# Optimization experiments

Hardware: AMD Instinct MI355X
Metric: run time of the kernel (lower is better)

Reference implementation:

```python
import jax, jax.numpy as jnp
import numpy as np
import math

B, L, D, H = 2, 2048, 1024, 16
d = D // H

def setup_inputs() -> dict:
    key = jax.random.key(0)
    ks = jax.random.split(key, 12)
    s = 0.02
    return {
        "x": jax.random.normal(ks[0], (B, L, D), jnp.float32),
        "Wqkv_w": jax.random.normal(ks[1], (D, 3 * D), jnp.float32) * s,
        "Wqkv_b": jax.random.normal(ks[2], (3 * D,), jnp.float32) * s,
        "out_w": jax.random.normal(ks[3], (D, D), jnp.float32) * s,
        "out_b": jax.random.normal(ks[4], (D,), jnp.float32) * s,
        "W_static": jnp.zeros((H, d, d), jnp.float32),
        "Lambda_raw": jax.random.uniform(ks[5], (H, d, d), jnp.float32, -3.0, 3.0),
        "Gamma": jax.random.uniform(ks[6], (H, d, d), jnp.float32, -0.5 / math.sqrt(d), 0.5 / math.sqrt(d)),
        "gate_w1": jax.random.normal(ks[7], (D, D // 2), jnp.float32) * s,
        "gate_b1": jax.random.normal(ks[8], (D // 2,), jnp.float32) * s,
        "gate_w2": jax.random.normal(ks[9], (D // 2, H), jnp.float32) * s,
        "gate_b2": jax.random.normal(ks[10], (H,), jnp.float32) * s,
    }

def _forward(x, Wqkv_w, Wqkv_b, out_w, out_b, W_static, Lambda_raw, Gamma,
             gate_w1, gate_b1, gate_w2, gate_b2):
    scale = 1.0 / math.sqrt(d)
    qkv = x @ Wqkv_w + Wqkv_b                              # (B,L,3D)
    qkv = qkv.reshape(B, L, 3, H, d).transpose(2, 0, 3, 1, 4)  # (3,B,H,L,d)
    q, k, v = qkv[0], qkv[1], qkv[2]

    # --- causal softmax attention branch ---
    scores = jnp.einsum('bhid,bhjd->bhij', q, k) * scale
    mask = jnp.triu(jnp.full((L, L), -10000.0, scores.dtype), 1)
    attn = jax.nn.softmax(scores + mask, axis=-1)
    y_softmax = jnp.einsum('bhij,bhjd->bhid', attn, v)     # (B,H,L,d)

    # --- STP fast-weight branch: decaying Hebbian state recurrence ---
    k_stp = k * scale
    retention = 1.0 - jax.nn.sigmoid(Lambda_raw)           # (H,d,d)
    def step(state, qkv_t):
        q_t, k_t, v_t = qkv_t                              # each (B,H,d)
        hebbian = v_t[..., :, None] * k_t[..., None, :]    # (B,H,d,d)
        state = retention * state + Gamma * hebbian
        y_t = jnp.einsum('bhij,bhj->bhi', W_static + state, q_t)
        return state, y_t
    qkv_seq = (q.transpose(2, 0, 1, 3), k_stp.transpose(2, 0, 1, 3), v.transpose(2, 0, 1, 3))
    state0 = jnp.zeros((B, H, d, d), x.dtype)
    _, y_stp = jax.lax.scan(step, state0, qkv_seq)         # (L,B,H,d)
    y_stp = y_stp.transpose(1, 2, 0, 3)                    # (B,H,L,d)

    # --- learned gate ---
    h = jax.nn.gelu(x @ gate_w1 + gate_b1, approximate=False)
    alpha = jax.nn.sigmoid(h @ gate_w2 + gate_b2)          # (B,L,H)
    alpha = alpha.transpose(0, 2, 1)[..., None]            # (B,H,L,1)

    y = alpha * y_softmax + (1.0 - alpha) * y_stp          # (B,H,L,d)
    y = y.transpose(0, 2, 1, 3).reshape(B, L, D)
    return y @ out_w + out_b

def reference(x, Wqkv_w, Wqkv_b, out_w, out_b, W_static, Lambda_raw, Gamma,
              gate_w1, gate_b1, gate_w2, gate_b2):
    return _forward(x, Wqkv_w, Wqkv_b, out_w, out_b, W_static, Lambda_raw, Gamma,
                    gate_w1, gate_b1, gate_w2, gate_b2)
```

## Files before the change

kernel.cpp:

```cpp
#include <hip/hip_runtime.h>
#include <cstdint>
#include <cstddef>

#define B_ 2
#define L_ 2048
#define D_ 1024
#define H_ 16
#define DH 64

typedef __attribute__((ext_vector_type(8))) short bf16x8;
typedef __attribute__((ext_vector_type(4))) float f32x4;
typedef unsigned short u16;

__device__ inline u16 f2bf(float f) {
  unsigned u = __builtin_bit_cast(unsigned, f);
  u += 0x7fffu + ((u >> 16) & 1u);
  return (u16)(u >> 16);
}

__device__ inline float bf2f(u16 x) {
  return __builtin_bit_cast(float, (unsigned)x << 16);
}

template <int CTRL>
__device__ inline float dpp_mov(float x) {
  int t = __builtin_amdgcn_update_dpp(0, __builtin_bit_cast(int, x), CTRL, 0xf, 0xf, true);
  return __builtin_bit_cast(float, t);
}

#define GLDS16(ldst, gsrc)                                              \
  __builtin_amdgcn_global_load_lds(                                    \
      (const __attribute__((address_space(1))) void*)(gsrc),           \
      (__attribute__((address_space(3))) void*)(ldst), 16, 0, 0)

__device__ inline void stp_upd(float4& z, const float4 r, const float4 g,
                               const float4 wlc, float vv,
                               float kx, float ky, float kz, float kw) {
  z.x = fmaf(r.x, z.x, fmaf(g.x * vv, kx, wlc.x));
  z.y = fmaf(r.y, z.y, fmaf(g.y * vv, ky, wlc.y));
  z.z = fmaf(r.z, z.z, fmaf(g.z * vv, kz, wlc.z));
  z.w = fmaf(r.w, z.w, fmaf(g.w * vv, kw, wlc.w));
}

__device__ inline void stp_upd1(float4& z, const float4 r, const float4 g,
                                float vv, float kx, float ky, float kz, float kw) {
  z.x = fmaf(r.x, z.x, (g.x * vv) * kx);
  z.y = fmaf(r.y, z.y, (g.y * vv) * ky);
  z.z = fmaf(r.z, z.z, (g.z * vv) * kz);
  z.w = fmaf(r.w, z.w, (g.w * vv) * kw);
}

__device__ inline float stp_dot(const float4 z, float qx, float qy, float qz, float qw) {
  float p = z.x * qx;
  p = fmaf(z.y, qy, p);
  p = fmaf(z.z, qz, p);
  p = fmaf(z.w, qw, p);
  return p;
}

__device__ inline float dpp_red16(float p) {
  p = p + dpp_mov<0x128>(p);
  p = p + dpp_mov<0x124>(p);
  p = p + dpp_mov<0x122>(p);
  p = p + dpp_mov<0x121>(p);
  return p;
}


__device__ inline void d_transpose(const float* __restrict__ in,
                                   u16* __restrict__ out, int R, int C,
                                   int bx, int by, float tile[32][33], int tid) {
  const int tx = tid & 31, ty = tid >> 5;
  const int c0 = bx * 32, r0 = by * 32;
#pragma unroll
  for (int j = 0; j < 4; ++j)
    tile[ty + j * 8][tx] = in[(size_t)(r0 + ty + j * 8) * C + c0 + tx];
  __syncthreads();
#pragma unroll
  for (int j = 0; j < 4; ++j)
    out[(size_t)(c0 + ty + j * 8) * R + r0 + tx] = f2bf(tile[tx][ty + j * 8]);
}

__global__ __launch_bounds__(256) void prep_fused(
    const float* __restrict__ x, u16* __restrict__ xbf,
    const float* __restrict__ wqkv_w, u16* __restrict__ wqkvT,
    const float* __restrict__ out_w, u16* __restrict__ owT,
    const float* __restrict__ g_w1, u16* __restrict__ g1T,
    const float* __restrict__ lam, const float* __restrict__ gma,
    float* __restrict__ retb, float* __restrict__ gamb,
    float* __restrict__ retb64) {
  __shared__ float tile[32][33];
  const int bid = blockIdx.x, tid = threadIdx.x;
  if (bid < 4096) {
    int i = bid * 256 + tid;
    float4 v = ((const float4*)x)[i];
    ushort4 o;
    o.x = f2bf(v.x); o.y = f2bf(v.y); o.z = f2bf(v.z); o.w = f2bf(v.w);
    ((ushort4*)xbf)[i] = o;
  } else if (bid < 7168) {
    int r = bid - 4096;
    d_transpose(wqkv_w, wqkvT, 1024, 3072, r % 96, r / 96, tile, tid);
  } else if (bid < 8192) {
    int r = bid - 7168;
    d_transpose(out_w, owT, 1024, 1024, r % 32, r / 32, tile, tid);
  } else if (bid < 8704) {
    int r = bid - 8192;
    d_transpose(g_w1, g1T, 1024, 512, r % 16, r / 16, tile, tid);
  } else {
    int i = (bid - 8704) * 256 + tid;
    float l = lam[i];
    float r = 1.f / (1.f + expf(l));
    retb[i] = r;
    gamb[i] = gma[i] * 0.125f;
    float r2 = r * r;
    float r4 = r2 * r2;
    float r8 = r4 * r4;
    float r16 = r8 * r8;
    float r32 = r16 * r16;
    retb64[i] = r32 * r32;
  }
}


struct GemmP {
  const u16* A; const u16* Bt; int M, N, K;
  const float* bias;
  u16* qb; u16* kb; u16* vtb;
  float* hout;
  float* outp;
};

template <int EPI>
__device__ void gemm_body(const GemmP& p, int lin0, int nwgx, int nwgtot,
                          u16* As, u16* Bs, u16* tileT) {
  const int tid = threadIdx.x;
  const int lane = tid & 63;
  const int w = tid >> 6;
  const int wr = w >> 1, wc = w & 1;
  const int lr = lane & 15, lk = lane >> 4;
  const int cpx = nwgtot >> 3;
  const int lin = (lin0 & 7) * cpx + (lin0 >> 3);
  const int m0 = (lin / nwgx) * 128, n0 = (lin % nwgx) * 128;

  f32x4 acc[4][4];
#pragma unroll
  for (int i = 0; i < 4; ++i)
#pragma unroll
    for (int j = 0; j < 4; ++j) acc[i][j] = (f32x4){0.f, 0.f, 0.f, 0.f};

  for (int k0 = 0; k0 < p.K; k0 += 64) {
    __syncthreads();
#pragma unroll
    for (int it = 0; it < 4; ++it) {
      int idx = it * 256 + tid;
      int row = idx >> 3;
      int ch = (idx & 7) ^ (row & 7);
      GLDS16(&As[idx * 8], p.A + (size_t)(m0 + row) * p.K + k0 + ch * 8);
      GLDS16(&Bs[idx * 8], p.Bt + (size_t)(n0 + row) * p.K + k0 + ch * 8);
    }
    __syncthreads();
#pragma unroll
    for (int kk = 0; kk < 2; ++kk) {
      const int slot = ((kk * 4 + lk) ^ (lr & 7)) * 8;
      bf16x8 af[4], bfr[4];
#pragma unroll
      for (int mr = 0; mr < 4; ++mr)
        af[mr] = *(const bf16x8*)&As[(wr * 64 + mr * 16 + lr) * 64 + slot];
#pragma unroll
      for (int nr = 0; nr < 4; ++nr)
        bfr[nr] = *(const bf16x8*)&Bs[(wc * 64 + nr * 16 + lr) * 64 + slot];
#pragma unroll
      for (int mr = 0; mr < 4; ++mr)
#pragma unroll
        for (int nr = 0; nr < 4; ++nr)
          acc[mr][nr] = __builtin_amdgcn_mfma_f32_16x16x32_bf16(af[mr], bfr[nr], acc[mr][nr], 0, 0, 0);
    }
  }

  if constexpr (EPI == 0) {
    if (n0 < 2048) {
#pragma unroll
      for (int mr = 0; mr < 4; ++mr)
#pragma unroll
        for (int nr = 0; nr < 4; ++nr) {
          const int col = n0 + wc * 64 + nr * 16 + lr;
#pragma unroll
          for (int rr = 0; rr < 4; ++rr) {
            const int row = m0 + wr * 64 + mr * 16 + lk * 4 + rr;
            float v = acc[mr][nr][rr] + p.bias[col];
            int which = col >> 10, hh = (col >> 6) & 15, ii = col & 63;
            int b = row >> 11, ll = row & 2047;
            size_t bi = ((size_t)(b * 16 + hh) * L_ + ll) * 64 + ii;
            if (which == 0) p.qb[bi] = f2bf(v * 0.125f);
            else            p.kb[bi] = f2bf(v);
          }
        }
    } else {
#pragma unroll 1
      for (int h2 = 0; h2 < 2; ++h2) {
        __syncthreads();
        if (wr == h2) {
#pragma unroll
          for (int mr = 0; mr < 4; ++mr)
#pragma unroll
            for (int nr = 0; nr < 4; ++nr) {
              const int cl = wc * 64 + nr * 16 + lr;
              const float bv = p.bias[n0 + cl];
#pragma unroll
              for (int rr = 0; rr < 4; ++rr) {
                const int rl2 = mr * 16 + lk * 4 + rr;
                tileT[cl * 72 + rl2] = f2bf(acc[mr][nr][rr] + bv);
              }
            }
        }
        __syncthreads();
        const int c = tid >> 1, half = tid & 1;
        const int vcol = (n0 - 2048) + c;
        const int hh = vcol >> 6, ii = vcol & 63;
        const int b = m0 >> 11;
        const int ll0 = (m0 & 2047) + h2 * 64 + half * 32;
        u16* dst = p.vtb + ((size_t)(b * 16 + hh) * 64 + ii) * L_ + ll0;
        const u16* src = &tileT[c * 72 + half * 32];
#pragma unroll
        for (int k = 0; k < 4; ++k)
          *(int4*)(dst + k * 8) = *(const int4*)(src + k * 8);
      }
    }
  } else {
#pragma unroll
    for (int mr = 0; mr < 4; ++mr)
#pragma unroll
      for (int nr = 0; nr < 4; ++nr) {
        const int col = n0 + wc * 64 + nr * 16 + lr;
#pragma unroll
        for (int rr = 0; rr < 4; ++rr) {
          const int row = m0 + wr * 64 + mr * 16 + lk * 4 + rr;
          float v = acc[mr][nr][rr] + p.bias[col];
          if constexpr (EPI == 1) {
            float g = 0.5f * v * (1.f + erff(v * 0.70710678118f));
            p.hout[(size_t)row * p.N + col] = g;
          } else {
            p.outp[(size_t)row * p.N + col] = v;
          }
        }
      }
  }
}

__global__ __launch_bounds__(256, 4) void gemm01_kernel(GemmP p0, GemmP p1) {
  __shared__ u16 sbuf[16384];
  u16* As = sbuf;
  u16* Bs = sbuf + 8192;
  u16* tileT = sbuf;
  const int bid = blockIdx.x;
  if (bid < 768) gemm_body<0>(p0, bid, 24, 768, As, Bs, tileT);
  else           gemm_body<1>(p1, bid - 768, 4, 128, As, Bs, tileT);
}

__global__ __launch_bounds__(256, 4) void gemm2_kernel(GemmP p) {
  __shared__ u16 As[8192];
  __shared__ u16 Bs[8192];
  const int lin0 = (int)blockIdx.x + 8 * (int)blockIdx.y;
  gemm_body<2>(p, lin0, 8, 256, As, Bs, nullptr);
}


__global__ __launch_bounds__(256) void alpha_kernel(
    const float* __restrict__ hbuf, const float* __restrict__ w2,
    const float* __restrict__ b2, float* __restrict__ alp) {
  const int tid = threadIdx.x;
  const int row = blockIdx.x * 16 + (tid >> 4);
  const int n = tid & 15;
  const float4* h4 = (const float4*)(hbuf + (size_t)row * 512);
  float acc = 0.f;
#pragma unroll 2
  for (int kk = 0; kk < 128; ++kk) {
    float4 hv = h4[kk];
    acc = fmaf(hv.x, w2[(kk * 4 + 0) * 16 + n], acc);
    acc = fmaf(hv.y, w2[(kk * 4 + 1) * 16 + n], acc);
    acc = fmaf(hv.z, w2[(kk * 4 + 2) * 16 + n], acc);
    acc = fmaf(hv.w, w2[(kk * 4 + 3) * 16 + n], acc);
  }
  float z = acc + b2[n];
  alp[row * 16 + n] = 1.f / (1.f + __expf(-z));
}


__global__ __launch_bounds__(256, 2) void attn_kernel(
    const u16* __restrict__ qb, const u16* __restrict__ kb,
    const u16* __restrict__ vtb, float* __restrict__ ysm) {
  __shared__ u16 Ks[64 * 64];
  __shared__ u16 Vts[64 * 64];
  __shared__ u16 Pl[4][16 * 64];
  const int tid = threadIdx.x, lane = tid & 63, w = tid >> 6;
  const int lr = lane & 15, lk = lane >> 4;
  const int lin = (int)blockIdx.x + 16 * (int)blockIdx.y;
  const int bh = lin & 31;
  const int xp = lin >> 5;
  const int qtA = 31 - xp, qtB = xp;

  const u16* kbase0 = kb + (size_t)bh * (L_ * 64);
  const u16* vbase0 = vtb + (size_t)bh * (64 * L_);

  const size_t qbaseA = ((size_t)bh * L_ + qtA * 64 + w * 16 + lr) * 64;
  const size_t qbaseB = ((size_t)bh * L_ + qtB * 64 + w * 16 + lr) * 64;
  bf16x8 qfrA[2], qfrB[2];
  qfrA[0] = *(const bf16x8*)(qb + qbaseA + lk * 8);
  qfrA[1] = *(const bf16x8*)(qb + qbaseA + 32 + lk * 8);
  qfrB[0] = *(const bf16x8*)(qb + qbaseB + lk * 8);
  qfrB[1] = *(const bf16x8*)(qb + qbaseB + 32 + lk * 8);

  f32x4 yaccA[4], yaccB[4];
  float mrowA[4], lrowA[4], mrowB[4], lrowB[4];
#pragma unroll
  for (int i = 0; i < 4; ++i) {
    yaccA[i] = (f32x4){0.f, 0.f, 0.f, 0.f};
    yaccB[i] = (f32x4){0.f, 0.f, 0.f, 0.f};
    mrowA[i] = -1e30f; mrowB[i] = -1e30f;
    lrowA[i] = 0.f;    lrowB[i] = 0.f;
  }

  auto process = [&](const bf16x8* qfr, f32x4* yacc, float* mrow, float* lrow,
                     bool maskTile) {
    f32x4 s[4];
#pragma unroll
    for (int f = 0; f < 4; ++f) {
      f32x4 sf = (f32x4){0.f, 0.f, 0.f, 0.f};
#pragma unroll
      for (int ss = 0; ss < 2; ++ss) {
        bf16x8 kfr = *(const bf16x8*)&Ks[(f * 16 + lr) * 64 +
                                         (((ss * 4 + lk) ^ (lr & 7)) * 8)];
        sf = __builtin_amdgcn_mfma_f32_16x16x32_bf16(qfr[ss], kfr, sf, 0, 0, 0);
      }
      s[f] = sf;
    }
    if (maskTile) {
#pragma unroll
      for (int f = 0; f < 4; ++f)
#pragma unroll
        for (int rr = 0; rr < 4; ++rr)
          if (f * 16 + lr > w * 16 + lk * 4 + rr) s[f][rr] = -1e30f;
    }
    float mx[4];
#pragma unroll
    for (int rr = 0; rr < 4; ++rr) {
      float m = fmaxf(fmaxf(s[0][rr], s[1][rr]), fmaxf(s[2][rr], s[3][rr]));
      m = fmaxf(m, dpp_mov<0x128>(m));
      m = fmaxf(m, dpp_mov<0x124>(m));
      m = fmaxf(m, dpp_mov<0x122>(m));
      m = fmaxf(m, dpp_mov<0x121>(m));
      mx[rr] = m;
    }
    bool need = (mx[0] > mrow[0] + 8.f) | (mx[1] > mrow[1] + 8.f) |
                (mx[2] > mrow[2] + 8.f) | (mx[3] > mrow[3] + 8.f);
    if (__any(need)) {
#pragma unroll
      for (int rr = 0; rr < 4; ++rr) {
        float mn = fmaxf(mrow[rr], mx[rr]);
        float c = __expf(mrow[rr] - mn);
        lrow[rr] *= c;
#pragma unroll
        for (int nf = 0; nf < 4; ++nf) yacc[nf][rr] *= c;
        mrow[rr] = mn;
      }
    }
    u16* pw = &Pl[w][0];
#pragma unroll
    for (int rr = 0; rr < 4; ++rr) {
      const int prow = lk * 4 + rr;
      float rs = 0.f;
#pragma unroll
      for (int f = 0; f < 4; ++f) {
        float pv = __expf(s[f][rr] - mrow[rr]);
        rs += pv;
        int chunk = f * 2 + (lr >> 3);
        pw[prow * 64 + ((chunk ^ (prow & 7)) * 8) + (lr & 7)] = f2bf(pv);
      }
      rs = rs + dpp_mov<0x128>(rs);
      rs = rs + dpp_mov<0x124>(rs);
      rs = rs + dpp_mov<0x122>(rs);
      rs = rs + dpp_mov<0x121>(rs);
      lrow[rr] += rs;
    }
#pragma unroll
    for (int s2 = 0; s2 < 2; ++s2) {
      bf16x8 pa = *(const bf16x8*)&pw[lr * 64 + (((s2 * 4 + lk) ^ (lr & 7)) * 8)];
#pragma unroll
      for (int nf = 0; nf < 4; ++nf) {
        bf16x8 vfr = *(const bf16x8*)&Vts[(nf * 16 + lr) * 64 +
                                          (((s2 * 4 + lk) ^ (lr & 7)) * 8)];
        yacc[nf] = __builtin_amdgcn_mfma_f32_16x16x32_bf16(pa, vfr, yacc[nf], 0, 0, 0);
      }
    }
  };

  const int nkv = qtA + 1;
  for (int kt = 0; kt < nkv; ++kt) {
    const int kv0 = kt * 64;
    __syncthreads();
#pragma unroll
    for (int it = 0; it < 2; ++it) {
      int idx = it * 256 + tid;
      int row = idx >> 3, ch = idx & 7;
      int sch = (ch ^ (row & 7)) * 8;
      *(int4*)&Ks[row * 64 + sch] =
          *(const int4*)(kbase0 + (size_t)(kv0 + row) * 64 + ch * 8);
      *(int4*)&Vts[row * 64 + sch] =
          *(const int4*)(vbase0 + (size_t)row * L_ + kv0 + ch * 8);
    }
    __syncthreads();

    process(qfrA, yaccA, mrowA, lrowA, kt == qtA);
    if (kt <= qtB) process(qfrB, yaccB, mrowB, lrowB, kt == qtB);
  }

#pragma unroll
  for (int nf = 0; nf < 4; ++nf)
#pragma unroll
    for (int rr = 0; rr < 4; ++rr) {
      int rowl = w * 16 + lk * 4 + rr;
      int col = nf * 16 + lr;
      ysm[((size_t)bh * L_ + qtA * 64 + rowl) * 64 + col] = yaccA[nf][rr] / lrowA[rr];
      ysm[((size_t)bh * L_ + qtB * 64 + rowl) * 64 + col] = yaccB[nf][rr] / lrowB[rr];
    }
}


__global__ __launch_bounds__(256, 4) void stp_pass1(
    const u16* __restrict__ kb, const u16* __restrict__ vtb,
    const float* __restrict__ retb, const float* __restrict__ gamb,
    float* __restrict__ slocal) {
  __shared__ u16 Klds[4096];
  const int tid = threadIdx.x, lane = tid & 63, w = tid >> 6;
  const int bh = blockIdx.x >> 5, c = blockIdx.x & 31;
  const int hh = bh & 15;
  const int m = lane >> 4, j4 = (lane & 15) * 4;
  const int i0m = w * 16 + m * 4;

  const u16* kcb = kb + ((size_t)bh * L_ + c * 64) * 64;
  GLDS16(&Klds[tid * 8], kcb + tid * 8);
  GLDS16(&Klds[2048 + tid * 8], kcb + 2048 + tid * 8);
  __syncthreads();

  const int hij = (hh * 64 + i0m) * 64 + j4;
  const float4 r0 = *(const float4*)(retb + hij);
  const float4 r1 = *(const float4*)(retb + hij + 64);
  const float4 r2 = *(const float4*)(retb + hij + 128);
  const float4 r3 = *(const float4*)(retb + hij + 192);
  const float4 g0 = *(const float4*)(gamb + hij);
  const float4 g1 = *(const float4*)(gamb + hij + 64);
  const float4 g2 = *(const float4*)(gamb + hij + 128);
  const float4 g3 = *(const float4*)(gamb + hij + 192);
  const u16* vbp = vtb + ((size_t)bh * 64 + i0m) * L_ + c * 64;

  float4 s0 = {0,0,0,0}, s1 = {0,0,0,0}, s2 = {0,0,0,0}, s3 = {0,0,0,0};
#pragma unroll 1
  for (int t8 = 0; t8 < 8; ++t8) {
    const bf16x8 va = *(const bf16x8*)(vbp + t8 * 8);
    const bf16x8 vb = *(const bf16x8*)(vbp + L_ + t8 * 8);
    const bf16x8 vc = *(const bf16x8*)(vbp + 2 * L_ + t8 * 8);
    const bf16x8 vd = *(const bf16x8*)(vbp + 3 * L_ + t8 * 8);
#pragma unroll
    for (int tt = 0; tt < 8; ++tt) {
      const ushort4 k4u = *(const ushort4*)&Klds[(t8 * 8 + tt) * 64 + j4];
      const float kx = bf2f(k4u.x), ky = bf2f(k4u.y),
                  kz = bf2f(k4u.z), kw = bf2f(k4u.w);
      stp_upd1(s0, r0, g0, bf2f((u16)va[tt]), kx, ky, kz, kw);
      stp_upd1(s1, r1, g1, bf2f((u16)vb[tt]), kx, ky, kz, kw);
      stp_upd1(s2, r2, g2, bf2f((u16)vc[tt]), kx, ky, kz, kw);
      stp_upd1(s3, r3, g3, bf2f((u16)vd[tt]), kx, ky, kz, kw);
    }
  }
  float* sb = slocal + (((size_t)(bh * 32 + c) * 64) + i0m) * 64 + j4;
  *(float4*)(sb)       = s0;
  *(float4*)(sb + 64)  = s1;
  *(float4*)(sb + 128) = s2;
  *(float4*)(sb + 192) = s3;
}

__global__ __launch_bounds__(256) void stp_scan(
    const float* __restrict__ retb64, float* __restrict__ slocal) {
  const int idx = blockIdx.x * 256 + threadIdx.x;
  const int j = idx & 63, i1 = (idx >> 6) & 63, bh = idx >> 12;
  const int hh = bh & 15;
  const float r64 = retb64[(hh * 64 + i1) * 64 + j];
  float carry = 0.f;
  for (int c = 0; c < 32; ++c) {
    const size_t off = ((((size_t)bh * 32 + c) * 64 + i1) * 64 + j);
    const float sl = slocal[off];
    slocal[off] = carry;
    carry = fmaf(r64, carry, sl);
  }
}

__global__ __launch_bounds__(256, 4) void stp_pass2(
    const u16* __restrict__ qb, const u16* __restrict__ kb,
    const u16* __restrict__ vtb, const float* __restrict__ retb,
    const float* __restrict__ gamb, const float* __restrict__ wst,
    const float* __restrict__ slocal, float* __restrict__ ystp) {
  __shared__ u16 KQ[8192];
  const int tid = threadIdx.x, lane = tid & 63, w = tid >> 6;
  const int bh = blockIdx.x >> 5, c = blockIdx.x & 31;
  const int hh = bh & 15;
  const int m = lane >> 4, jc = lane & 15, j4 = jc * 4;
  const int i0m = w * 16 + m * 4;

  const size_t cb = ((size_t)bh * L_ + c * 64) * 64;
  GLDS16(&KQ[tid * 8], kb + cb + tid * 8);
  GLDS16(&KQ[2048 + tid * 8], kb + cb + 2048 + tid * 8);
  GLDS16(&KQ[4096 + tid * 8], qb + cb + tid * 8);
  GLDS16(&KQ[6144 + tid * 8], qb + cb + 2048 + tid * 8);
  __syncthreads();

  const int hij = (hh * 64 + i0m) * 64 + j4;
  const float4 r0 = *(const float4*)(retb + hij);
  const float4 r1 = *(const float4*)(retb + hij + 64);
  const float4 r2 = *(const float4*)(retb + hij + 128);
  const float4 r3 = *(const float4*)(retb + hij + 192);
  const float4 g0 = *(const float4*)(gamb + hij);
  const float4 g1 = *(const float4*)(gamb + hij + 64);
  const float4 g2 = *(const float4*)(gamb + hij + 128);
  const float4 g3 = *(const float4*)(gamb + hij + 192);
  const float4 w0 = *(const float4*)(wst + hij);
  const float4 w1 = *(const float4*)(wst + hij + 64);
  const float4 w2 = *(const float4*)(wst + hij + 128);
  const float4 w3 = *(const float4*)(wst + hij + 192);

  const float* sb = slocal + (((size_t)(bh * 32 + c) * 64) + i0m) * 64 + j4;
  float4 z0 = *(const float4*)(sb);
  float4 z1 = *(const float4*)(sb + 64);
  float4 z2 = *(const float4*)(sb + 128);
  float4 z3 = *(const float4*)(sb + 192);

  float4 wlc0, wlc1, wlc2, wlc3;
  wlc0.x = w0.x * (1.f - r0.x); wlc0.y = w0.y * (1.f - r0.y);
  wlc0.z = w0.z * (1.f - r0.z); wlc0.w = w0.w * (1.f - r0.w);
  wlc1.x = w1.x * (1.f - r1.x); wlc1.y = w1.y * (1.f - r1.y);
  wlc1.z = w1.z * (1.f - r1.z); wlc1.w = w1.w * (1.f - r1.w);
  wlc2.x = w2.x * (1.f - r2.x); wlc2.y = w2.y * (1.f - r2.y);
  wlc2.z = w2.z * (1.f - r2.z); wlc2.w = w2.w * (1.f - r2.w);
  wlc3.x = w3.x * (1.f - r3.x); wlc3.y = w3.y * (1.f - r3.y);
  wlc3.z = w3.z * (1.f - r3.z); wlc3.w = w3.w * (1.f - r3.w);
  z0.x += w0.x; z0.y += w0.y; z0.z += w0.z; z0.w += w0.w;
  z1.x += w1.x; z1.y += w1.y; z1.z += w1.z; z1.w += w1.w;
  z2.x += w2.x; z2.y += w2.y; z2.z += w2.z; z2.w += w2.w;
  z3.x += w3.x; z3.y += w3.y; z3.z += w3.z; z3.w += w3.w;

  const u16* vbp = vtb + ((size_t)bh * 64 + i0m) * L_ + c * 64;
  float* yp = ystp + cb + i0m;

#pragma unroll 1
  for (int t8 = 0; t8 < 8; ++t8) {
    const bf16x8 va = *(const bf16x8*)(vbp + t8 * 8);
    const bf16x8 vb = *(const bf16x8*)(vbp + L_ + t8 * 8);
    const bf16x8 vc = *(const bf16x8*)(vbp + 2 * L_ + t8 * 8);
    const bf16x8 vd = *(const bf16x8*)(vbp + 3 * L_ + t8 * 8);
#pragma unroll
    for (int tt = 0; tt < 8; ++tt) {
      const int t = t8 * 8 + tt;
      const ushort4 k4u = *(const ushort4*)&KQ[t * 64 + j4];
      const ushort4 q4u = *(const ushort4*)&KQ[4096 + t * 64 + j4];
      const float kx = bf2f(k4u.x), ky = bf2f(k4u.y),
                  kz = bf2f(k4u.z), kw = bf2f(k4u.w);
      const float qx = bf2f(q4u.x), qy = bf2f(q4u.y),
                  qz = bf2f(q4u.z), qw = bf2f(q4u.w);
      stp_upd(z0, r0, g0, wlc0, bf2f((u16)va[tt]), kx, ky, kz, kw);
      stp_upd(z1, r1, g1, wlc1, bf2f((u16)vb[tt]), kx, ky, kz, kw);
      stp_upd(z2, r2, g2, wlc2, bf2f((u16)vc[tt]), kx, ky, kz, kw);
      stp_upd(z3, r3, g3, wlc3, bf2f((u16)vd[tt]), kx, ky, kz, kw);
      float p0 = dpp_red16(stp_dot(z0, qx, qy, qz, qw));
      float p1 = dpp_red16(stp_dot(z1, qx, qy, qz, qw));
      float p2 = dpp_red16(stp_dot(z2, qx, qy, qz, qw));
      float p3 = dpp_red16(stp_dot(z3, qx, qy, qz, qw));
      if (jc == 0) {
        float4 yo;
        yo.x = p0 * 8.f; yo.y = p1 * 8.f; yo.z = p2 * 8.f; yo.w = p3 * 8.f;
        *(float4*)(yp + t * 64) = yo;
      }
    }
  }
}


__global__ __launch_bounds__(256) void blend_kernel(
    const float* __restrict__ ysm, const float* __restrict__ ystp,
    const float* __restrict__ alp, u16* __restrict__ ycomb) {
  int idx = blockIdx.x * 256 + threadIdx.x;
  int m = idx >> 8;
  int n4 = (idx & 255) * 4;
  int hh = n4 >> 6, ii = n4 & 63;
  int b = m >> 11, ll = m & 2047;
  size_t bi = ((size_t)(b * 16 + hh) * L_ + ll) * 64 + ii;
  float a = alp[m * 16 + hh];
  float4 s = *(const float4*)(ysm + bi);
  float4 t = *(const float4*)(ystp + bi);
  ushort4 o;
  o.x = f2bf(a * s.x + (1.f - a) * t.x);
  o.y = f2bf(a * s.y + (1.f - a) * t.y);
  o.z = f2bf(a * s.z + (1.f - a) * t.z);
  o.w = f2bf(a * s.w + (1.f - a) * t.w);
  *(ushort4*)(ycomb + (size_t)m * 1024 + n4) = o;
}


extern "C" void kernel_launch(void* const* d_in, const int* in_sizes, int n_in,
                              void* d_out, int out_size, void* d_ws, size_t ws_size,
                              hipStream_t stream) {
  const float* x       = (const float*)d_in[0];
  const float* wqkv_w  = (const float*)d_in[1];
  const float* wqkv_b  = (const float*)d_in[2];
  const float* out_w   = (const float*)d_in[3];
  const float* out_b   = (const float*)d_in[4];
  const float* w_stat  = (const float*)d_in[5];
  const float* lam     = (const float*)d_in[6];
  const float* gma     = (const float*)d_in[7];
  const float* g_w1    = (const float*)d_in[8];
  const float* g_b1    = (const float*)d_in[9];
  const float* g_w2    = (const float*)d_in[10];
  const float* g_b2    = (const float*)d_in[11];

  char* ws = (char*)d_ws;
  size_t off = 0;
  auto nxt = [&](size_t b) { size_t r = off; off += (b + 255) & ~(size_t)255; return r; };
  u16*   xbf   = (u16*)(ws + nxt((size_t)4096 * 1024 * 2));
  u16*   wqkvT = (u16*)(ws + nxt((size_t)3072 * 1024 * 2));
  u16*   owT   = (u16*)(ws + nxt((size_t)1024 * 1024 * 2));
  u16*   g1T   = (u16*)(ws + nxt((size_t)512 * 1024 * 2));
  u16*   qb    = (u16*)(ws + nxt((size_t)4194304 * 2));
  u16*   kb    = (u16*)(ws + nxt((size_t)4194304 * 2));
  u16*   vtb   = (u16*)(ws + nxt((size_t)4194304 * 2));
  float* ysm   = (float*)(ws + nxt((size_t)4194304 * 4));
  float* ystp  = (float*)(ws + nxt((size_t)4194304 * 4));
  size_t hbuf_off = nxt((size_t)4096 * 512 * 4);
  float* hbuf  = (float*)(ws + hbuf_off);
  u16*   ycomb = (u16*)(ws + nxt((size_t)4096 * 1024 * 2));
  float* slocal = (float*)(ws + hbuf_off);
  float* alp   = (float*)(ws + nxt((size_t)4096 * 16 * 4));
  float* retb  = (float*)(ws + nxt((size_t)65536 * 4));
  float* gamb  = (float*)(ws + nxt((size_t)65536 * 4));
  float* retb64= (float*)(ws + nxt((size_t)65536 * 4));

  dim3 blk(256);
  prep_fused<<<8960, blk, 0, stream>>>(x, xbf, wqkv_w, wqkvT, out_w, owT,
                                       g_w1, g1T, lam, gma, retb, gamb, retb64);

  GemmP p0 = {xbf, wqkvT, 4096, 3072, 1024, wqkv_b,
              qb, kb, vtb, nullptr, nullptr};
  GemmP p1 = {xbf, g1T, 4096, 512, 1024, g_b1,
              nullptr, nullptr, nullptr, hbuf, nullptr};
  gemm01_kernel<<<896, blk, 0, stream>>>(p0, p1);

  alpha_kernel<<<256, blk, 0, stream>>>(hbuf, g_w2, g_b2, alp);

  attn_kernel<<<dim3(16, 32), blk, 0, stream>>>(qb, kb, vtb, ysm);

  stp_pass1<<<1024, blk, 0, stream>>>(kb, vtb, retb, gamb, slocal);
  stp_scan<<<512, blk, 0, stream>>>(retb64, slocal);
  stp_pass2<<<1024, blk, 0, stream>>>(qb, kb, vtb, retb, gamb, w_stat,
                                      slocal, ystp);

  blend_kernel<<<4096, blk, 0, stream>>>(ysm, ystp, alp, ycomb);

  GemmP p2 = {ycomb, owT, 4096, 1024, 1024, out_b,
              nullptr, nullptr, nullptr, nullptr, (float*)d_out};
  gemm2_kernel<<<dim3(8, 32), blk, 0, stream>>>(p2);
}
```

Baseline: 245.6 us.

## Split attention KV range across two blocks and merge partials in blend

Replaces the paired-query-tile attention schedule with a split-KV scheme. Each block now handles one query tile over half of its causal KV range, giving 2048 blocks instead of 512. Each block writes an unnormalized partial output plus its row max and row sum, and the blend kernel combines the two halves with a log-sum-exp rescale before gating. This is meant to raise occupancy and parallelism in attention. In exchange it doubles the fp32 partial-output traffic, leaves per-block work uneven, and K/V tile loads are no longer shared between two query tiles.

```diff
diff --git a/kernel.cpp b/kernel.cpp
--- a/kernel.cpp
+++ b/kernel.cpp
@@ -288,40 +288,54 @@
 
 __global__ __launch_bounds__(256, 2) void attn_kernel(
     const u16* __restrict__ qb, const u16* __restrict__ kb,
-    const u16* __restrict__ vtb, float* __restrict__ ysm) {
+    const u16* __restrict__ vtb, float* __restrict__ osm,
+    float* __restrict__ mlb) {
   __shared__ u16 Ks[64 * 64];
   __shared__ u16 Vts[64 * 64];
   __shared__ u16 Pl[4][16 * 64];
   const int tid = threadIdx.x, lane = tid & 63, w = tid >> 6;
   const int lr = lane & 15, lk = lane >> 4;
-  const int lin = (int)blockIdx.x + 16 * (int)blockIdx.y;
+  const int lin = (int)blockIdx.x;
   const int bh = lin & 31;
-  const int xp = lin >> 5;
-  const int qtA = 31 - xp, qtB = xp;
+  const int rest = lin >> 5;
+  const int qt = 31 - (rest >> 1);
+  const int half = rest & 1;
+  const int hs = (qt + 2) >> 1;
+  const int kt0 = half ? hs : 0;
+  const int kt1 = half ? (qt + 1) : hs;
 
   const u16* kbase0 = kb + (size_t)bh * (L_ * 64);
   const u16* vbase0 = vtb + (size_t)bh * (64 * L_);
 
-  const size_t qbaseA = ((size_t)bh * L_ + qtA * 64 + w * 16 + lr) * 64;
-  const size_t qbaseB = ((size_t)bh * L_ + qtB * 64 + w * 16 + lr) * 64;
-  bf16x8 qfrA[2], qfrB[2];
-  qfrA[0] = *(const bf16x8*)(qb + qbaseA + lk * 8);
-  qfrA[1] = *(const bf16x8*)(qb + qbaseA + 32 + lk * 8);
-  qfrB[0] = *(const bf16x8*)(qb + qbaseB + lk * 8);
-  qfrB[1] = *(const bf16x8*)(qb + qbaseB + 32 + lk * 8);
-
-  f32x4 yaccA[4], yaccB[4];
-  float mrowA[4], lrowA[4], mrowB[4], lrowB[4];
+  const size_t qbase = ((size_t)bh * L_ + qt * 64 + w * 16 + lr) * 64;
+  bf16x8 qfr[2];
+  qfr[0] = *(const bf16x8*)(qb + qbase + lk * 8);
+  qfr[1] = *(const bf16x8*)(qb + qbase + 32 + lk * 8);
+
+  f32x4 yacc[4];
+  float mrow[4], lrow[4];
 #pragma unroll
   for (int i = 0; i < 4; ++i) {
-    yaccA[i] = (f32x4){0.f, 0.f, 0.f, 0.f};
-    yaccB[i] = (f32x4){0.f, 0.f, 0.f, 0.f};
-    mrowA[i] = -1e30f; mrowB[i] = -1e30f;
-    lrowA[i] = 0.f;    lrowB[i] = 0.f;
-  }
-
-  auto process = [&](const bf16x8* qfr, f32x4* yacc, float* mrow, float* lrow,
-                     bool maskTile) {
+    yacc[i] = (f32x4){0.f, 0.f, 0.f, 0.f};
+    mrow[i] = -1e30f;
+    lrow[i] = 0.f;
+  }
+
+  for (int kt = kt0; kt < kt1; ++kt) {
+    const int kv0 = kt * 64;
+    __syncthreads();
+#pragma unroll
+    for (int it = 0; it < 2; ++it) {
+      int idx = it * 256 + tid;
+      int row = idx >> 3, ch = idx & 7;
+      int sch = (ch ^ (row & 7)) * 8;
+      *(int4*)&Ks[row * 64 + sch] =
+          *(const int4*)(kbase0 + (size_t)(kv0 + row) * 64 + ch * 8);
+      *(int4*)&Vts[row * 64 + sch] =
+          *(const int4*)(vbase0 + (size_t)row * L_ + kv0 + ch * 8);
+    }
+    __syncthreads();
+
     f32x4 s[4];
 #pragma unroll
     for (int f = 0; f < 4; ++f) {
@@ -334,7 +348,7 @@
       }
       s[f] = sf;
     }
-    if (maskTile) {
+    if (kt == qt) {
 #pragma unroll
       for (int f = 0; f < 4; ++f)
 #pragma unroll
@@ -392,37 +406,25 @@
         yacc[nf] = __builtin_amdgcn_mfma_f32_16x16x32_bf16(pa, vfr, yacc[nf], 0, 0, 0);
       }
     }
-  };
-
-  const int nkv = qtA + 1;
-  for (int kt = 0; kt < nkv; ++kt) {
-    const int kv0 = kt * 64;
-    __syncthreads();
-#pragma unroll
-    for (int it = 0; it < 2; ++it) {
-      int idx = it * 256 + tid;
-      int row = idx >> 3, ch = idx & 7;
-      int sch = (ch ^ (row & 7)) * 8;
-      *(int4*)&Ks[row * 64 + sch] =
-          *(const int4*)(kbase0 + (size_t)(kv0 + row) * 64 + ch * 8);
-      *(int4*)&Vts[row * 64 + sch] =
-          *(const int4*)(vbase0 + (size_t)row * L_ + kv0 + ch * 8);
-    }
-    __syncthreads();
-
-    process(qfrA, yaccA, mrowA, lrowA, kt == qtA);
-    if (kt <= qtB) process(qfrB, yaccB, mrowB, lrowB, kt == qtB);
-  }
-
+  }
+
+  float* obase = osm + (size_t)half * 4194304;
 #pragma unroll
   for (int nf = 0; nf < 4; ++nf)
 #pragma unroll
     for (int rr = 0; rr < 4; ++rr) {
       int rowl = w * 16 + lk * 4 + rr;
       int col = nf * 16 + lr;
-      ysm[((size_t)bh * L_ + qtA * 64 + rowl) * 64 + col] = yaccA[nf][rr] / lrowA[rr];
-      ysm[((size_t)bh * L_ + qtB * 64 + rowl) * 64 + col] = yaccB[nf][rr] / lrowB[rr];
-    }
+      obase[((size_t)bh * L_ + qt * 64 + rowl) * 64 + col] = yacc[nf][rr];
+    }
+  if (lr == 0) {
+    const int rbase = bh * L_ + qt * 64 + w * 16 + lk * 4;
+#pragma unroll
+    for (int rr = 0; rr < 4; ++rr) {
+      mlb[half * 131072 + rbase + rr] = mrow[rr];
+      mlb[half * 131072 + 65536 + rbase + rr] = lrow[rr];
+    }
+  }
 }
 
 
@@ -583,22 +585,31 @@
 
 
 __global__ __launch_bounds__(256) void blend_kernel(
-    const float* __restrict__ ysm, const float* __restrict__ ystp,
-    const float* __restrict__ alp, u16* __restrict__ ycomb) {
+    const float* __restrict__ osm, const float* __restrict__ mlb,
+    const float* __restrict__ ystp, const float* __restrict__ alp,
+    u16* __restrict__ ycomb) {
   int idx = blockIdx.x * 256 + threadIdx.x;
   int m = idx >> 8;
   int n4 = (idx & 255) * 4;
   int hh = n4 >> 6, ii = n4 & 63;
   int b = m >> 11, ll = m & 2047;
-  size_t bi = ((size_t)(b * 16 + hh) * L_ + ll) * 64 + ii;
+  const int bh = b * 16 + hh;
+  size_t bi = ((size_t)bh * L_ + ll) * 64 + ii;
+  const int rowg = bh * L_ + ll;
+  float m1 = mlb[rowg],          l1 = mlb[65536 + rowg];
+  float m2 = mlb[131072 + rowg], l2 = mlb[196608 + rowg];
+  float mm = fmaxf(m1, m2);
+  float e1 = __expf(m1 - mm), e2 = __expf(m2 - mm);
+  float inv = 1.f / (l1 * e1 + l2 * e2);
+  float4 o1 = *(const float4*)(osm + bi);
+  float4 o2 = *(const float4*)(osm + 4194304 + bi);
   float a = alp[m * 16 + hh];
-  float4 s = *(const float4*)(ysm + bi);
   float4 t = *(const float4*)(ystp + bi);
   ushort4 o;
-  o.x = f2bf(a * s.x + (1.f - a) * t.x);
-  o.y = f2bf(a * s.y + (1.f - a) * t.y);
-  o.z = f2bf(a * s.z + (1.f - a) * t.z);
-  o.w = f2bf(a * s.w + (1.f - a) * t.w);
+  o.x = f2bf(a * ((o1.x * e1 + o2.x * e2) * inv) + (1.f - a) * t.x);
+  o.y = f2bf(a * ((o1.y * e1 + o2.y * e2) * inv) + (1.f - a) * t.y);
+  o.z = f2bf(a * ((o1.z * e1 + o2.z * e2) * inv) + (1.f - a) * t.z);
+  o.w = f2bf(a * ((o1.w * e1 + o2.w * e2) * inv) + (1.f - a) * t.w);
   *(ushort4*)(ycomb + (size_t)m * 1024 + n4) = o;
 }
 
@@ -629,7 +640,8 @@
   u16*   qb    = (u16*)(ws + nxt((size_t)4194304 * 2));
   u16*   kb    = (u16*)(ws + nxt((size_t)4194304 * 2));
   u16*   vtb   = (u16*)(ws + nxt((size_t)4194304 * 2));
-  float* ysm   = (float*)(ws + nxt((size_t)4194304 * 4));
+  float* osm   = (float*)(ws + nxt((size_t)2 * 4194304 * 4));
+  float* mlb   = (float*)(ws + nxt((size_t)4 * 65536 * 4));
   float* ystp  = (float*)(ws + nxt((size_t)4194304 * 4));
   size_t hbuf_off = nxt((size_t)4096 * 512 * 4);
   float* hbuf  = (float*)(ws + hbuf_off);
@@ -652,14 +664,14 @@
 
   alpha_kernel<<<256, blk, 0, stream>>>(hbuf, g_w2, g_b2, alp);
 
-  attn_kernel<<<dim3(16, 32), blk, 0, stream>>>(qb, kb, vtb, ysm);
+  attn_kernel<<<2048, blk, 0, stream>>>(qb, kb, vtb, osm, mlb);
 
   stp_pass1<<<1024, blk, 0, stream>>>(kb, vtb, retb, gamb, slocal);
   stp_scan<<<512, blk, 0, stream>>>(retb64, slocal);
   stp_pass2<<<1024, blk, 0, stream>>>(qb, kb, vtb, retb, gamb, w_stat,
                                       slocal, ystp);
 
-  blend_kernel<<<4096, blk, 0, stream>>>(ysm, ystp, alp, ycomb);
+  blend_kernel<<<4096, blk, 0, stream>>>(osm, mlb, ystp, alp, ycomb);
 
   GemmP p2 = {ycomb, owT, 4096, 1024, 1024, out_b,
               nullptr, nullptr, nullptr, nullptr, (float*)d_out};
```

Result: no change. 241.9 us (-1.5%).
